# Optimization experiments

Measured on AMD Instinct MI355X. Metric: run time of the kernel, lower is better.

Reference implementation:

```python
import jax, jax.numpy as jnp
import numpy as np

B, T, I, H = 2048, 256, 64, 64  # batch, seq_len, input_size, hidden_size


def setup_inputs() -> dict:
    key = jax.random.key(0)
    ks = jax.random.split(key, 11)
    w = lambda k, shape: (jax.random.normal(k, shape, jnp.float32) * 0.05)
    return {
        "x": jax.random.normal(ks[0], (B, T, I), jnp.float32),
        # layer 0 (input -> hidden), PyTorch gate order [i, f, g, o] stacked along dim 0
        "W_ih0": w(ks[1], (4 * H, I)),
        "W_hh0": w(ks[2], (4 * H, H)),
        "b_ih0": w(ks[3], (4 * H,)),
        "b_hh0": w(ks[4], (4 * H,)),
        # layer 1 (hidden -> hidden)
        "W_ih1": w(ks[5], (4 * H, H)),
        "W_hh1": w(ks[6], (4 * H, H)),
        "b_ih1": w(ks[7], (4 * H,)),
        "b_hh1": w(ks[8], (4 * H,)),
        # final projection hidden -> 1
        "fc_w": w(ks[9], (1, H)),
        "fc_b": w(ks[10], (1,)),
    }


def _lstm_layer(x, W_ih, W_hh, b_ih, b_hh):
    """Single LSTM layer, batch_first input (B, T, D) -> (B, T, H).
    PyTorch gate order: i, f, g, o."""
    Bsz, Tlen, _ = x.shape
    Hd = W_hh.shape[1]
    # Precompute input projections for all timesteps in one big GEMM.
    x_proj = jnp.einsum("btd,gd->btg", x, W_ih) + b_ih + b_hh  # (B, T, 4H)
    x_proj = jnp.swapaxes(x_proj, 0, 1)  # (T, B, 4H) for scan over time

    def step(carry, xt):
        h, c = carry
        gates = xt + h @ W_hh.T  # (B, 4H)
        i, f, g, o = jnp.split(gates, 4, axis=-1)
        i = jax.nn.sigmoid(i)
        f = jax.nn.sigmoid(f)
        g = jnp.tanh(g)
        o = jax.nn.sigmoid(o)
        c = f * c + i * g
        h = o * jnp.tanh(c)
        return (h, c), h

    h0 = jnp.zeros((Bsz, Hd), x.dtype)
    (_, _), hs = jax.lax.scan(step, (h0, h0), x_proj)
    return jnp.swapaxes(hs, 0, 1)  # (B, T, H)


def reference(x, W_ih0, W_hh0, b_ih0, b_hh0, W_ih1, W_hh1, b_ih1, b_hh1, fc_w, fc_b):
    # Dropout between layers is inactive in eval mode -> omitted.
    h1 = _lstm_layer(x, W_ih0, W_hh0, b_ih0, b_hh0)
    h2 = _lstm_layer(h1, W_ih1, W_hh1, b_ih1, b_hh1)
    last_hidden = h2[:, -1, :]  # (B, H)
    out = last_hidden @ fc_w.T + fc_b  # (B, 1)
    return out[:, 0]  # squeeze(-1) -> (B,)
```

## Files before the change

kernel.cpp:

```cpp
#include <hip/hip_runtime.h>

typedef short short8 __attribute__((ext_vector_type(8)));
typedef float f32x4  __attribute__((ext_vector_type(4)));
typedef unsigned short u16;

#define T_LEN 256
#define NB    8
#define GRID  (2048 / NB)
#define LDK   72

static __device__ __forceinline__ u16 bf16_rne(float f) {
    unsigned u = __builtin_bit_cast(unsigned, f);
    return (u16)((u + 0x7fffu + ((u >> 16) & 1u)) >> 16);
}
static __device__ __forceinline__ float bf16_f(u16 h) {
    unsigned u = ((unsigned)h) << 16;
    return __builtin_bit_cast(float, u);
}
static __device__ __forceinline__ void split_tr(float f, u16& hi, u16& lo) {
    unsigned u = __builtin_bit_cast(unsigned, f);
    hi = (u16)(u >> 16);
    float rest = f - __builtin_bit_cast(float, u & 0xffff0000u);
    lo = (u16)(__builtin_bit_cast(unsigned, rest) >> 16);
}
static __device__ __forceinline__ float fast_sigmoid(float x) {
    float e = __builtin_amdgcn_exp2f(x * -1.4426950408889634f);
    return __builtin_amdgcn_rcpf(1.0f + e);
}
static __device__ __forceinline__ float fast_tanh(float x) {
    float e = __builtin_amdgcn_exp2f(x * -2.8853900817779268f);
    return 2.0f * __builtin_amdgcn_rcpf(1.0f + e) - 1.0f;
}

__global__ __launch_bounds__(1024)
void lstm2_mfma(const float* __restrict__ x,
                const float* __restrict__ W_ih0, const float* __restrict__ W_hh0,
                const float* __restrict__ b_ih0, const float* __restrict__ b_hh0,
                const float* __restrict__ W_ih1, const float* __restrict__ W_hh1,
                const float* __restrict__ b_ih1, const float* __restrict__ b_hh1,
                const float* __restrict__ fc_w,  const float* __restrict__ fc_b,
                float* __restrict__ out)
{
    const int tid = threadIdx.x;
    const int l   = tid & 63;
    const int w   = tid >> 6;
    const int grp = w >> 3;
    const int wl  = w & 7;
    const int ln  = l & 15;
    const int kg  = l >> 4;

    __shared__ __align__(16) u16 XB[2][16][LDK];
    __shared__ __align__(16) u16 H1[2][16][LDK];
    __shared__ __align__(16) u16 H2[2][16][LDK];
    __shared__ __align__(16) float hfin[NB][68];

    short8 Ah[2][4], Al[2][4];
    f32x4  biasv[2];
    {
        const float* Wi = grp ? W_ih1 : W_ih0;
        const float* Wh = grp ? W_hh1 : W_hh0;
        const float* bi = grp ? b_ih1 : b_ih0;
        const float* bh = grp ? b_hh1 : b_hh0;
        #pragma unroll
        for (int mt = 0; mt < 2; ++mt) {
            #pragma unroll
            for (int kt = 0; kt < 4; ++kt) {
                const int uu   = ln >> 2;
                const int gate = ln & 3;
                const int row  = gate * 64 + (wl * 8 + mt * 4 + uu);
                const int kb   = kt * 32 + kg * 8;
                const float* src = (kb < 64) ? (Wi + (size_t)row * 64 + kb)
                                             : (Wh + (size_t)row * 64 + (kb - 64));
                short8 h8, l8;
                #pragma unroll
                for (int j = 0; j < 8; ++j) {
                    float v = src[j];
                    u16 hh = bf16_rne(v);
                    u16 ll = bf16_rne(v - bf16_f(hh));
                    h8[j] = (short)hh; l8[j] = (short)ll;
                }
                Ah[mt][kt] = h8; Al[mt][kt] = l8;
            }
            f32x4 bv;
            #pragma unroll
            for (int r = 0; r < 4; ++r) {
                const int row = r * 64 + (wl * 8 + mt * 4 + kg);
                bv[r] = bi[row] + bh[row];
            }
            biasv[mt] = bv;
        }
    }

    {
        u16* p0 = &XB[0][0][0];
        u16* p1 = &H1[0][0][0];
        u16* p2 = &H2[0][0][0];
        const int tot = 2 * 16 * LDK;
        for (int i = tid; i < tot; i += 1024) { p0[i] = 0; p1[i] = 0; p2[i] = 0; }
    }
    __syncthreads();

    const int    sb    = blockIdx.x * NB;
    const int    xs    = (tid >> 6) & 7;
    const int    xj    = tid & 63;
    const bool   stg   = (tid < 512);
    const size_t xbase = ((size_t)(sb + xs)) * T_LEN * 64 + xj;

    if (stg) {
        u16 hh, ll; split_tr(x[xbase], hh, ll);
        XB[0][xs][xj]     = hh;
        XB[0][8 + xs][xj] = ll;
    }
    __syncthreads();

    const int  mtl  = (ln >> 3) & 1;
    const int  smp  = ln & 7;
    const int  un   = wl * 8 + mtl * 4 + kg;
    const bool lo8  = (ln < 8);
    float cstate = 0.f;
    float xcur = stg ? x[xbase + 64] : 0.f;

#define MFMA(A, B, C) __builtin_amdgcn_mfma_f32_16x16x32_bf16(A, B, C, 0, 0, 0)

#define STEPB(T, G0, G1, STG_ON, XLOAD, FIN)                                 \
    do {                                                                     \
        const int p_ = (T) & 1, q_ = p_ ^ 1;                                 \
        float xnext_ = 0.f;                                                  \
        if ((XLOAD) && stg) xnext_ = x[xbase + (size_t)((T) + 2) * 64];      \
        const bool act_ = grp ? (bool)(G1) : (bool)(G0);                     \
        if (act_) {                                                          \
            const u16 (*BA)[LDK] = grp ? H1[p_] : XB[p_];                    \
            const u16 (*BB)[LDK] = grp ? H2[p_] : H1[p_];                    \
            short8 b0 = *(const short8*)&BA[ln][kg * 8];                     \
            short8 b1 = *(const short8*)&BA[ln][32 + kg * 8];                \
            short8 b2 = *(const short8*)&BB[ln][kg * 8];                     \
            short8 b3 = *(const short8*)&BB[ln][32 + kg * 8];                \
            f32x4 aH0 = {0.f,0.f,0.f,0.f}, aH1 = {0.f,0.f,0.f,0.f};          \
            f32x4 aL0 = biasv[0],          aL1 = biasv[1];                   \
            aH0 = MFMA(Ah[0][0], b0, aH0);  aH1 = MFMA(Ah[1][0], b0, aH1);   \
            aL0 = MFMA(Al[0][0], b0, aL0);  aL1 = MFMA(Al[1][0], b0, aL1);   \
            aH0 = MFMA(Ah[0][1], b1, aH0);  aH1 = MFMA(Ah[1][1], b1, aH1);   \
            aL0 = MFMA(Al[0][1], b1, aL0);  aL1 = MFMA(Al[1][1], b1, aL1);   \
            aH0 = MFMA(Ah[0][2], b2, aH0);  aH1 = MFMA(Ah[1][2], b2, aH1);   \
            aL0 = MFMA(Al[0][2], b2, aL0);  aL1 = MFMA(Al[1][2], b2, aL1);   \
            aH0 = MFMA(Ah[0][3], b3, aH0);  aH1 = MFMA(Ah[1][3], b3, aH1);   \
            aL0 = MFMA(Al[0][3], b3, aL0);  aL1 = MFMA(Al[1][3], b3, aL1);   \
            f32x4 pk;                                                        \
            _Pragma("unroll")                                                \
            for (int r = 0; r < 4; ++r) {                                    \
                float u1_   = aH1[r] + aL1[r];                     \
                float send_ = lo8 ? u1_ : aH0[r];             \
                int   si_   = __builtin_bit_cast(int, send_);                \
                int   ri_   = __builtin_amdgcn_mov_dpp(si_, 0x128, 0xf, 0xf, \
                                                       true);     \
                float recv_ = __builtin_bit_cast(float, ri_);                \
                pk[r] = lo8 ? (aH0[r] + recv_ + aL0[r]) : (aH1[r] + recv_);  \
            }                                                                \
            const float ig = fast_sigmoid(pk[0]);                            \
            const float fg = fast_sigmoid(pk[1]);                            \
            const float gg = fast_tanh(pk[2]);                               \
            const float og = fast_sigmoid(pk[3]);                            \
            const float cc = fg * cstate + ig * gg;                          \
            cstate = cc;                                                     \
            const float hv = og * fast_tanh(cc);                             \
            u16 hh_, ll_; split_tr(hv, hh_, ll_);                            \
            if (grp == 0) {                                                  \
                H1[q_][smp][un]     = hh_;                                   \
                H1[q_][8 + smp][un] = ll_;                                   \
            } else {                                                         \
                H2[q_][smp][un]     = hh_;                                   \
                H2[q_][8 + smp][un] = ll_;                                   \
                if (FIN) hfin[smp][un] = hv;                                 \
            }                                                                \
        }                                                                    \
        if ((STG_ON) && stg) {                                               \
            u16 hh_, ll_; split_tr(xcur, hh_, ll_);                          \
            XB[q_][xs][xj]     = hh_;                                        \
            XB[q_][8 + xs][xj] = ll_;                                        \
        }                                                                    \
        xcur = xnext_;                                                       \
        __syncthreads();                                                     \
    } while (0)

    STEPB(0, 1, 0, 1, 1, 0);
    #pragma unroll 1
    for (int t = 1; t <= 253; ++t) {
        STEPB(t, 1, 1, 1, 1, 0);
    }
    STEPB(254, 1, 1, 1, 0, 0);
    STEPB(255, 1, 1, 0, 0, 0);
    STEPB(256, 0, 1, 0, 0, 1);
#undef STEPB
#undef MFMA

    if (w < 8) {
        float v = hfin[w][l] * fc_w[l];
        #pragma unroll
        for (int off = 32; off; off >>= 1) v += __shfl_xor(v, off, 64);
        if (l == 0) out[sb + w] = v + fc_b[0];
    }
}

extern "C" void kernel_launch(void* const* d_in, const int* in_sizes, int n_in,
                              void* d_out, int out_size, void* d_ws, size_t ws_size,
                              hipStream_t stream) {
    const float* x     = (const float*)d_in[0];
    const float* W_ih0 = (const float*)d_in[1];
    const float* W_hh0 = (const float*)d_in[2];
    const float* b_ih0 = (const float*)d_in[3];
    const float* b_hh0 = (const float*)d_in[4];
    const float* W_ih1 = (const float*)d_in[5];
    const float* W_hh1 = (const float*)d_in[6];
    const float* b_ih1 = (const float*)d_in[7];
    const float* b_hh1 = (const float*)d_in[8];
    const float* fc_w  = (const float*)d_in[9];
    const float* fc_b  = (const float*)d_in[10];
    float* out = (float*)d_out;

    lstm2_mfma<<<GRID, 1024, 0, stream>>>(x, W_ih0, W_hh0, b_ih0, b_hh0,
                                          W_ih1, W_hh1, b_ih1, b_hh1,
                                          fc_w, fc_b, out);
}
```

Baseline: 266.2 us.

## Merge MFMA accumulators, unroll time loop by two, move x staging to layer-1 waves

The hi and lo MFMA products now share one accumulator per tile, and the bias is folded into the initial value only on lanes that keep their own half. This cuts four accumulators to two and removes the extra adds before the DPP exchange. The time loop is unrolled by two so the ping-pong buffer index is a compile-time constant, which removes index arithmetic and pointer selection. Staging of x into shared memory moves from the first 512 threads to the layer-1 wave group. This rebalances work away from the layer-0 group, but changes which threads issue the global loads.

```diff
diff --git a/kernel.cpp b/kernel.cpp
--- a/kernel.cpp
+++ b/kernel.cpp
@@ -101,9 +101,9 @@
     __syncthreads();
 
     const int    sb    = blockIdx.x * NB;
-    const int    xs    = (tid >> 6) & 7;
-    const int    xj    = tid & 63;
-    const bool   stg   = (tid < 512);
+    const bool   stg   = (grp == 1);
+    const int    xs    = wl;
+    const int    xj    = l;
     const size_t xbase = ((size_t)(sb + xs)) * T_LEN * 64 + xj;
 
     if (stg) {
@@ -117,44 +117,51 @@
     const int  smp  = ln & 7;
     const int  un   = wl * 8 + mtl * 4 + kg;
     const bool lo8  = (ln < 8);
+    const f32x4 zv  = {0.f, 0.f, 0.f, 0.f};
+    const f32x4 init0 = lo8 ? biasv[0] : zv;
+    const f32x4 init1 = lo8 ? biasv[1] : zv;
     float cstate = 0.f;
     float xcur = stg ? x[xbase + 64] : 0.f;
 
 #define MFMA(A, B, C) __builtin_amdgcn_mfma_f32_16x16x32_bf16(A, B, C, 0, 0, 0)
 
-#define STEPB(T, G0, G1, STG_ON, XLOAD, FIN)                                 \
+#define STEPB(T, P, G0, G1, STG_ON, XLOAD, FIN)                              \
     do {                                                                     \
-        const int p_ = (T) & 1, q_ = p_ ^ 1;                                 \
         float xnext_ = 0.f;                                                  \
         if ((XLOAD) && stg) xnext_ = x[xbase + (size_t)((T) + 2) * 64];      \
         const bool act_ = grp ? (bool)(G1) : (bool)(G0);                     \
         if (act_) {                                                          \
-            const u16 (*BA)[LDK] = grp ? H1[p_] : XB[p_];                    \
-            const u16 (*BB)[LDK] = grp ? H2[p_] : H1[p_];                    \
-            short8 b0 = *(const short8*)&BA[ln][kg * 8];                     \
-            short8 b1 = *(const short8*)&BA[ln][32 + kg * 8];                \
-            short8 b2 = *(const short8*)&BB[ln][kg * 8];                     \
-            short8 b3 = *(const short8*)&BB[ln][32 + kg * 8];                \
-            f32x4 aH0 = {0.f,0.f,0.f,0.f}, aH1 = {0.f,0.f,0.f,0.f};          \
-            f32x4 aL0 = biasv[0],          aL1 = biasv[1];                   \
-            aH0 = MFMA(Ah[0][0], b0, aH0);  aH1 = MFMA(Ah[1][0], b0, aH1);   \
-            aL0 = MFMA(Al[0][0], b0, aL0);  aL1 = MFMA(Al[1][0], b0, aL1);   \
-            aH0 = MFMA(Ah[0][1], b1, aH0);  aH1 = MFMA(Ah[1][1], b1, aH1);   \
-            aL0 = MFMA(Al[0][1], b1, aL0);  aL1 = MFMA(Al[1][1], b1, aL1);   \
-            aH0 = MFMA(Ah[0][2], b2, aH0);  aH1 = MFMA(Ah[1][2], b2, aH1);   \
-            aL0 = MFMA(Al[0][2], b2, aL0);  aL1 = MFMA(Al[1][2], b2, aL1);   \
-            aH0 = MFMA(Ah[0][3], b3, aH0);  aH1 = MFMA(Ah[1][3], b3, aH1);   \
-            aL0 = MFMA(Al[0][3], b3, aL0);  aL1 = MFMA(Al[1][3], b3, aL1);   \
+            short8 b0, b1, b2, b3;                                           \
+            if (grp) {                                                       \
+                b0 = *(const short8*)&H1[P][ln][kg * 8];                     \
+                b1 = *(const short8*)&H1[P][ln][32 + kg * 8];                \
+                b2 = *(const short8*)&H2[P][ln][kg * 8];                     \
+                b3 = *(const short8*)&H2[P][ln][32 + kg * 8];                \
+            } else {                                                         \
+                b0 = *(const short8*)&XB[P][ln][kg * 8];                     \
+                b1 = *(const short8*)&XB[P][ln][32 + kg * 8];                \
+                b2 = *(const short8*)&H1[P][ln][kg * 8];                     \
+                b3 = *(const short8*)&H1[P][ln][32 + kg * 8];                \
+            }                                                                \
+            f32x4 a0 = init0, a1 = init1;                                    \
+            a0 = MFMA(Ah[0][0], b0, a0);  a1 = MFMA(Ah[1][0], b0, a1);       \
+            a0 = MFMA(Al[0][0], b0, a0);  a1 = MFMA(Al[1][0], b0, a1);       \
+            a0 = MFMA(Ah[0][1], b1, a0);  a1 = MFMA(Ah[1][1], b1, a1);       \
+            a0 = MFMA(Al[0][1], b1, a0);  a1 = MFMA(Al[1][1], b1, a1);       \
+            a0 = MFMA(Ah[0][2], b2, a0);  a1 = MFMA(Ah[1][2], b2, a1);       \
+            a0 = MFMA(Al[0][2], b2, a0);  a1 = MFMA(Al[1][2], b2, a1);       \
+            a0 = MFMA(Ah[0][3], b3, a0);  a1 = MFMA(Ah[1][3], b3, a1);       \
+            a0 = MFMA(Al[0][3], b3, a0);  a1 = MFMA(Al[1][3], b3, a1);       \
             f32x4 pk;                                                        \
             _Pragma("unroll")                                                \
             for (int r = 0; r < 4; ++r) {                                    \
-                float u1_   = aH1[r] + aL1[r];                     \
-                float send_ = lo8 ? u1_ : aH0[r];             \
+                float send_ = lo8 ? a1[r] : a0[r];            \
                 int   si_   = __builtin_bit_cast(int, send_);                \
                 int   ri_   = __builtin_amdgcn_mov_dpp(si_, 0x128, 0xf, 0xf, \
                                                        true);     \
                 float recv_ = __builtin_bit_cast(float, ri_);                \
-                pk[r] = lo8 ? (aH0[r] + recv_ + aL0[r]) : (aH1[r] + recv_);  \
+                float self_ = lo8 ? a0[r] : a1[r];                           \
+                pk[r] = self_ + recv_;                                       \
             }                                                                \
             const float ig = fast_sigmoid(pk[0]);                            \
             const float fg = fast_sigmoid(pk[1]);                            \
@@ -165,31 +172,33 @@
             const float hv = og * fast_tanh(cc);                             \
             u16 hh_, ll_; split_tr(hv, hh_, ll_);                            \
             if (grp == 0) {                                                  \
-                H1[q_][smp][un]     = hh_;                                   \
-                H1[q_][8 + smp][un] = ll_;                                   \
+                H1[1 - (P)][smp][un]     = hh_;                              \
+                H1[1 - (P)][8 + smp][un] = ll_;                              \
             } else {                                                         \
-                H2[q_][smp][un]     = hh_;                                   \
-                H2[q_][8 + smp][un] = ll_;                                   \
+                H2[1 - (P)][smp][un]     = hh_;                              \
+                H2[1 - (P)][8 + smp][un] = ll_;                              \
                 if (FIN) hfin[smp][un] = hv;                                 \
             }                                                                \
         }                                                                    \
         if ((STG_ON) && stg) {                                               \
             u16 hh_, ll_; split_tr(xcur, hh_, ll_);                          \
-            XB[q_][xs][xj]     = hh_;                                        \
-            XB[q_][8 + xs][xj] = ll_;                                        \
+            XB[1 - (P)][xs][xj]     = hh_;                                   \
+            XB[1 - (P)][8 + xs][xj] = ll_;                                   \
         }                                                                    \
         xcur = xnext_;                                                       \
         __syncthreads();                                                     \
     } while (0)
 
-    STEPB(0, 1, 0, 1, 1, 0);
+    STEPB(0, 0, 1, 0, 1, 1, 0);
     #pragma unroll 1
-    for (int t = 1; t <= 253; ++t) {
-        STEPB(t, 1, 1, 1, 1, 0);
-    }
-    STEPB(254, 1, 1, 1, 0, 0);
-    STEPB(255, 1, 1, 0, 0, 0);
-    STEPB(256, 0, 1, 0, 0, 1);
+    for (int t = 1; t <= 251; t += 2) {
+        STEPB(t,     1, 1, 1, 1, 1, 0);
+        STEPB(t + 1, 0, 1, 1, 1, 1, 0);
+    }
+    STEPB(253, 1, 1, 1, 1, 1, 0);
+    STEPB(254, 0, 1, 1, 1, 0, 0);
+    STEPB(255, 1, 1, 1, 0, 0, 0);
+    STEPB(256, 0, 0, 1, 0, 0, 1);
 #undef STEPB
 #undef MFMA
 
```

After: 238.5 us. -10.4%, faster.
